# Kernel optimization log

Measured on AMD Instinct MI355X. Metric: run time of the kernel, lower is better.

Reference implementation:

```python
import jax, jax.numpy as jnp
import numpy as np

GRID_SIZE = 5
SPLINE_ORDER = 3
GRID_RANGE = (-1.0, 1.0)
BN_EPS = 1e-5


def _make_grid():
    h = (GRID_RANGE[1] - GRID_RANGE[0]) / GRID_SIZE
    # grid_size + 2*spline_order + 1 = 12 knots, shared across the 9 patch features
    return jnp.arange(-SPLINE_ORDER, GRID_SIZE + SPLINE_ORDER + 1, dtype=jnp.float32) * h + GRID_RANGE[0]


def _b_splines(x, grid):
    # x: (N, F) -> (N, F, grid_size + spline_order) via Cox-de Boor recursion
    x = x[..., None]
    bases = ((x >= grid[:-1]) & (x < grid[1:])).astype(x.dtype)
    for k in range(1, SPLINE_ORDER + 1):
        left = (x - grid[: -(k + 1)]) / (grid[k:-1] - grid[: -(k + 1)]) * bases[..., :-1]
        right = (grid[k + 1:] - x) / (grid[k + 1:] - grid[1:-k]) * bases[..., 1:]
        bases = left + right
    return bases


def setup_inputs() -> dict:
    key = jax.random.key(0)
    ks = jax.random.split(key, 4)
    B, C, H, W = 4, 64, 96, 96
    return {
        "x": jax.random.normal(ks[0], (B, C, H, W), dtype=jnp.float32),
        "base_weight": jax.random.normal(ks[1], (1, 9), dtype=jnp.float32) * 0.3,
        "spline_weight": jax.random.normal(ks[2], (1, 9, GRID_SIZE + SPLINE_ORDER), dtype=jnp.float32) * 0.3,
        "spline_scaler": jax.random.normal(ks[3], (1, 9), dtype=jnp.float32) * 0.3 + 1.0,
        "bn_gamma": jnp.ones((C,), dtype=jnp.float32),
        "bn_beta": jnp.zeros((C,), dtype=jnp.float32),
    }


def reference(x, base_weight, spline_weight, spline_scaler, bn_gamma, bn_beta):
    B, C, H, W = x.shape
    grid = _make_grid()
    # Per-channel depthwise 3x3 patch extraction (pad 1, stride 1), shared KANLinear(9 -> 1)
    patches = jax.lax.conv_general_dilated_patches(
        x.reshape(B * C, 1, H, W), (3, 3), (1, 1), [(1, 1), (1, 1)]
    )  # (B*C, 9, H, W)
    tok = patches.transpose(0, 2, 3, 1).reshape(-1, 9)  # (N, 9)

    base_out = jax.nn.silu(tok) @ base_weight.T  # (N, 1)
    bases = _b_splines(tok, grid)  # (N, 9, 8)
    scaled_sw = (spline_weight * spline_scaler[..., None]).reshape(1, -1)  # (1, 72)
    spline_out = bases.reshape(tok.shape[0], -1) @ scaled_sw.T  # (N, 1)

    y = (base_out + spline_out).reshape(B, C, H, W)

    # BatchNorm2d (training-mode batch statistics) + ReLU
    mean = y.mean(axis=(0, 2, 3))
    var = y.var(axis=(0, 2, 3))
    y_hat = (y - mean[None, :, None, None]) * jax.lax.rsqrt(var + BN_EPS)[None, :, None, None]
    out = jax.nn.relu(y_hat * bn_gamma[None, :, None, None] + bn_beta[None, :, None, None])
    return out
```

## Files before the change

kernel.cpp:

```cpp
#include <hip/hip_runtime.h>
#include <math.h>

#define HH 96
#define WW 96
#define CC 64
#define BB 4
#define PLANE (HH * WW)
#define NPLANES (BB * CC)
#define NPC (BB * PLANE)
#define TILE 32
#define TPL 3
#define NTILES (TPL * TPL)
#define HALO 34
#define HALO_N (HALO * HALO)
#define BLOCK 256

typedef _Float16 h2v __attribute__((ext_vector_type(2)));

static __device__ __forceinline__ float dot2h(unsigned a, unsigned b, float c) {
#if __has_builtin(__builtin_amdgcn_fdot2)
    return __builtin_amdgcn_fdot2(__builtin_bit_cast(h2v, a),
                                  __builtin_bit_cast(h2v, b), c, false);
#else
    h2v x = __builtin_bit_cast(h2v, a);
    h2v y = __builtin_bit_cast(h2v, b);
    return c + (float)x[0] * (float)y[0] + (float)x[1] * (float)y[1];
#endif
}

static __device__ __forceinline__ unsigned pk16(float a, float b) {
    return __builtin_bit_cast(unsigned, __builtin_amdgcn_cvt_pkrtz(a, b));
}


__global__ __launch_bounds__(BLOCK) void kconv_stage1(
    const float* __restrict__ x,
    const float* __restrict__ base_w,
    const float* __restrict__ spline_w,
    const float* __restrict__ spline_s,
    float* __restrict__ y,
    float2* __restrict__ part)
{
    __shared__ uint4  s_n[2][HALO_N];
    __shared__ float  s_sl[2][HALO_N];
    __shared__ unsigned s_wp[36];
    __shared__ float  s_bw[9];
    __shared__ float2 red[4];

    const int tid = threadIdx.x;

    if (tid < 36) {
        const int j = tid >> 2;
        const int k = tid & 3;
        const float sc = spline_s[j];
        s_wp[tid] = pk16(spline_w[j * 8 + 2 * k] * sc,
                         spline_w[j * 8 + 2 * k + 1] * sc);
    }
    if (tid < 9) s_bw[tid] = base_w[tid];

    const int plane = blockIdx.y;
    const int h0 = blockIdx.x * TILE;
    const float* xp = x + (size_t)plane * PLANE;

    int hy[5], hx[5];
#pragma unroll
    for (int s = 0; s < 5; ++s) {
        const int i = tid + s * BLOCK;
        const int r = i / HALO;
        hy[s] = r;
        hx[s] = i - r * HALO;
    }

    const int tx  = tid & 31;
    const int ty4 = (tid >> 5) * 4;

    float lsum = 0.0f, lsq = 0.0f;

    float v[5];
#pragma unroll
    for (int s = 0; s < 5; ++s) {
        const int gh = h0 + hy[s] - 1;
        const int gw = hx[s] - 1;
        const bool ok = (tid + s * BLOCK < HALO_N) &&
                        gh >= 0 && gh < HH && gw >= 0 && gw < WW;
        v[s] = ok ? xp[gh * WW + gw] : 0.0f;
    }
#pragma unroll
    for (int s = 0; s < 5; ++s) {
        const int i = tid + s * BLOCK;
        if (i >= HALO_N) break;
        const float vv = v[s];
        const float e  = __expf(-vv);
        const float sl = vv * __builtin_amdgcn_rcpf(1.0f + e);
        const float sp = fmaf(vv, 2.5f, 2.5f);
        const float tf = floorf(sp);
        const float u  = sp - tf;
        const int   t  = (int)tf;
        const int   m  = t >> 1;
        const bool  odd = (t & 1) != 0;
        const float w1m = 1.0f - u;
        const float u2 = u * u;
        const float u3 = u2 * u;
        const float B0 = w1m * w1m * (w1m * (1.0f / 6.0f));
        const float B3 = u2 * (u * (1.0f / 6.0f));
        const float B1 = fmaf(-u2, 1.0f, fmaf(u3, 0.5f, 2.0f / 3.0f));
        const float B2 = 1.0f - B0 - B1 - B3;
        const unsigned h01 = pk16(B0, B1);
        const unsigned h23 = pk16(B2, B3);
        unsigned n[4];
        unsigned a_prev;
        {
            const int k0 = -1 - m;
            a_prev = (k0 == 0) ? h01 : ((k0 == 1) ? h23 : 0u);
        }
#pragma unroll
        for (int d = 0; d < 4; ++d) {
            const int k0 = d - m;
            const unsigned a_cur = (k0 == 0) ? h01 : ((k0 == 1) ? h23 : 0u);
            const unsigned sh = __builtin_amdgcn_alignbit(a_cur, a_prev, 16);
            n[d] = odd ? sh : a_cur;
            a_prev = a_cur;
        }
        s_n[0][i]  = make_uint4(n[0], n[1], n[2], n[3]);
        s_sl[0][i] = sl;
    }
    __syncthreads();

    unsigned wp[36];
    float bw[9];
#pragma unroll
    for (int q = 0; q < 36; ++q)
        wp[q] = __builtin_amdgcn_readfirstlane(s_wp[q]);
#pragma unroll
    for (int q = 0; q < 9; ++q)
        bw[q] = __int_as_float(__builtin_amdgcn_readfirstlane(__float_as_int(s_bw[q])));

#pragma unroll
    for (int wt = 0; wt < TPL; ++wt) {
        const int cur = wt & 1;
        const int nxt = cur ^ 1;

        if (wt < TPL - 1) {
            const int w0n = (wt + 1) * TILE;
#pragma unroll
            for (int s = 0; s < 5; ++s) {
                const int gh = h0 + hy[s] - 1;
                const int gw = w0n + hx[s] - 1;
                const bool ok = (tid + s * BLOCK < HALO_N) &&
                                gh >= 0 && gh < HH && gw >= 0 && gw < WW;
                v[s] = ok ? xp[gh * WW + gw] : 0.0f;
            }
        }

        float acc[4] = {0.0f, 0.0f, 0.0f, 0.0f};
#pragma unroll
        for (int r = 0; r < 6; ++r) {
            const int base = (ty4 + r) * HALO + tx;
            uint4 cn[3];
            float cs[3];
#pragma unroll
            for (int dw = 0; dw < 3; ++dw) {
                cn[dw] = s_n[cur][base + dw];
                cs[dw] = s_sl[cur][base + dw];
            }
#pragma unroll
            for (int k = 0; k < 4; ++k) {
                const int dh = r - k;
                if (dh >= 0 && dh < 3) {
                    float a = acc[k];
#pragma unroll
                    for (int dw = 0; dw < 3; ++dw) {
                        const int j = dh * 3 + dw;
                        a = dot2h(cn[dw].x, wp[j * 4 + 0], a);
                        a = dot2h(cn[dw].y, wp[j * 4 + 1], a);
                        a = dot2h(cn[dw].z, wp[j * 4 + 2], a);
                        a = dot2h(cn[dw].w, wp[j * 4 + 3], a);
                        a = fmaf(bw[j], cs[dw], a);
                    }
                    acc[k] = a;
                }
            }
        }

        float* yp = y + (size_t)plane * PLANE + (size_t)h0 * WW + wt * TILE;
#pragma unroll
        for (int k = 0; k < 4; ++k) {
            yp[(ty4 + k) * WW + tx] = acc[k];
            lsum += acc[k];
            lsq = fmaf(acc[k], acc[k], lsq);
        }

        if (wt < TPL - 1) {
#pragma unroll
            for (int s = 0; s < 5; ++s) {
                const int i = tid + s * BLOCK;
                if (i >= HALO_N) break;
                const float vv = v[s];
                const float e  = __expf(-vv);
                const float sl = vv * __builtin_amdgcn_rcpf(1.0f + e);
                const float sp = fmaf(vv, 2.5f, 2.5f);
                const float tf = floorf(sp);
                const float u  = sp - tf;
                const int   t  = (int)tf;
                const int   m  = t >> 1;
                const bool  odd = (t & 1) != 0;
                const float w1m = 1.0f - u;
                const float u2 = u * u;
                const float u3 = u2 * u;
                const float B0 = w1m * w1m * (w1m * (1.0f / 6.0f));
                const float B3 = u2 * (u * (1.0f / 6.0f));
                const float B1 = fmaf(-u2, 1.0f, fmaf(u3, 0.5f, 2.0f / 3.0f));
                const float B2 = 1.0f - B0 - B1 - B3;
                const unsigned h01 = pk16(B0, B1);
                const unsigned h23 = pk16(B2, B3);
                unsigned n[4];
                unsigned a_prev;
                {
                    const int k0 = -1 - m;
                    a_prev = (k0 == 0) ? h01 : ((k0 == 1) ? h23 : 0u);
                }
#pragma unroll
                for (int d = 0; d < 4; ++d) {
                    const int k0 = d - m;
                    const unsigned a_cur = (k0 == 0) ? h01 : ((k0 == 1) ? h23 : 0u);
                    const unsigned sh = __builtin_amdgcn_alignbit(a_cur, a_prev, 16);
                    n[d] = odd ? sh : a_cur;
                    a_prev = a_cur;
                }
                s_n[nxt][i]  = make_uint4(n[0], n[1], n[2], n[3]);
                s_sl[nxt][i] = sl;
            }
            __syncthreads();
        }
    }

#pragma unroll
    for (int off = 32; off; off >>= 1) {
        lsum += __shfl_down(lsum, off, 64);
        lsq  += __shfl_down(lsq,  off, 64);
    }
    if ((tid & 63) == 0) red[tid >> 6] = make_float2(lsum, lsq);
    __syncthreads();
    if (tid == 0) {
        const float s = red[0].x + red[1].x + red[2].x + red[3].x;
        const float q = red[0].y + red[1].y + red[2].y + red[3].y;
        part[plane * NTILES + blockIdx.x] = make_float2(s, q);
    }
}

__global__ __launch_bounds__(BLOCK) void kconv_stage2(
    float* __restrict__ y,
    const float2* __restrict__ part,
    const float* __restrict__ gamma,
    const float* __restrict__ beta)
{
    __shared__ float2 sb;
    const int tid = threadIdx.x;
    const int plane = blockIdx.x;
    const int c = plane & (CC - 1);

    if (tid < 64) {
        float s = 0.0f, q = 0.0f;
        if (tid < 12) {
            const int b = tid / 3;
            const int t = tid - b * 3;
            const float2 pp = part[(c + CC * b) * NTILES + t];
            s = pp.x; q = pp.y;
        }
#pragma unroll
        for (int off = 8; off; off >>= 1) {
            s += __shfl_down(s, off, 64);
            q += __shfl_down(q, off, 64);
        }
        if (tid == 0) {
            const float inv = 1.0f / (float)NPC;
            const float mean = s * inv;
            const float var  = q * inv - mean * mean;
            const float sc   = rsqrtf(var + 1e-5f) * gamma[c];
            sb = make_float2(sc, beta[c] - mean * sc);
        }
    }
    __syncthreads();
    const float2 sbv = sb;

    float4* yp = (float4*)(y + (size_t)plane * PLANE + (size_t)blockIdx.y * 1024);
    float4 v = yp[tid];
    v.x = fmaxf(fmaf(v.x, sbv.x, sbv.y), 0.0f);
    v.y = fmaxf(fmaf(v.y, sbv.x, sbv.y), 0.0f);
    v.z = fmaxf(fmaf(v.z, sbv.x, sbv.y), 0.0f);
    v.w = fmaxf(fmaf(v.w, sbv.x, sbv.y), 0.0f);
    yp[tid] = v;
}

extern "C" void kernel_launch(void* const* d_in, const int* in_sizes, int n_in,
                              void* d_out, int out_size, void* d_ws, size_t ws_size,
                              hipStream_t stream)
{
    const float* x        = (const float*)d_in[0];
    const float* base_w   = (const float*)d_in[1];
    const float* spline_w = (const float*)d_in[2];
    const float* spline_s = (const float*)d_in[3];
    const float* gamma    = (const float*)d_in[4];
    const float* beta     = (const float*)d_in[5];
    float* out   = (float*)d_out;
    float2* part = (float2*)d_ws;

    dim3 g1(TPL, NPLANES);
    kconv_stage1<<<g1, BLOCK, 0, stream>>>(x, base_w, spline_w, spline_s, out, part);

    dim3 g2(NPLANES, PLANE / (BLOCK * 4));
    kconv_stage2<<<g2, BLOCK, 0, stream>>>(out, part, gamma, beta);
}
```

Measured before the change: 86.07 us.

## Fuse conv and batchnorm stages with grid-wide atomic barrier, keeping outputs in registers

Merges the two kernels into one persistent launch. Each block keeps its computed tile values in registers, publishes partial sums, and spins on a global atomic counter until all 768 blocks arrive. It then applies the batchnorm scale and shift plus ReLU and writes the output once. This removes the intermediate y write and re-read plus a kernel launch, but adds a memset launch and relies on all blocks being co-resident, with a spin timeout that could give wrong results if they are not.

```diff
diff --git a/kernel.cpp b/kernel.cpp
--- a/kernel.cpp
+++ b/kernel.cpp
@@ -10,10 +10,10 @@
 #define NPC (BB * PLANE)
 #define TILE 32
 #define TPL 3
-#define NTILES (TPL * TPL)
 #define HALO 34
 #define HALO_N (HALO * HALO)
 #define BLOCK 256
+#define NBLK (TPL * NPLANES)
 
 typedef _Float16 h2v __attribute__((ext_vector_type(2)));
 
@@ -33,19 +33,23 @@
 }
 
 
-__global__ __launch_bounds__(BLOCK) void kconv_stage1(
+__global__ __launch_bounds__(BLOCK, 3) void kconv_fused(
     const float* __restrict__ x,
     const float* __restrict__ base_w,
     const float* __restrict__ spline_w,
     const float* __restrict__ spline_s,
-    float* __restrict__ y,
-    float2* __restrict__ part)
+    const float* __restrict__ gamma,
+    const float* __restrict__ beta,
+    float* __restrict__ out,
+    float2* __restrict__ part,
+    unsigned* __restrict__ bar)
 {
     __shared__ uint4  s_n[2][HALO_N];
     __shared__ float  s_sl[2][HALO_N];
     __shared__ unsigned s_wp[36];
     __shared__ float  s_bw[9];
     __shared__ float2 red[4];
+    __shared__ float2 sb;
 
     const int tid = threadIdx.x;
 
@@ -75,6 +79,7 @@
     const int ty4 = (tid >> 5) * 4;
 
     float lsum = 0.0f, lsq = 0.0f;
+    float accAll[TPL][4];
 
     float v[5];
 #pragma unroll
@@ -182,10 +187,9 @@
             }
         }
 
-        float* yp = y + (size_t)plane * PLANE + (size_t)h0 * WW + wt * TILE;
 #pragma unroll
         for (int k = 0; k < 4; ++k) {
-            yp[(ty4 + k) * WW + tx] = acc[k];
+            accAll[wt][k] = acc[k];
             lsum += acc[k];
             lsq = fmaf(acc[k], acc[k], lsq);
         }
@@ -241,30 +245,35 @@
     }
     if ((tid & 63) == 0) red[tid >> 6] = make_float2(lsum, lsq);
     __syncthreads();
+
     if (tid == 0) {
         const float s = red[0].x + red[1].x + red[2].x + red[3].x;
         const float q = red[0].y + red[1].y + red[2].y + red[3].y;
-        part[plane * NTILES + blockIdx.x] = make_float2(s, q);
-    }
-}
-
-__global__ __launch_bounds__(BLOCK) void kconv_stage2(
-    float* __restrict__ y,
-    const float2* __restrict__ part,
-    const float* __restrict__ gamma,
-    const float* __restrict__ beta)
-{
-    __shared__ float2 sb;
-    const int tid = threadIdx.x;
-    const int plane = blockIdx.x;
+        const float2 pv = make_float2(s, q);
+        __hip_atomic_store((unsigned long long*)&part[plane * TPL + blockIdx.x],
+                           __builtin_bit_cast(unsigned long long, pv),
+                           __ATOMIC_RELAXED, __HIP_MEMORY_SCOPE_AGENT);
+        __hip_atomic_fetch_add(bar, 1u, __ATOMIC_RELEASE,
+                               __HIP_MEMORY_SCOPE_AGENT);
+        int spins = 0;
+        while (__hip_atomic_load(bar, __ATOMIC_ACQUIRE,
+                                 __HIP_MEMORY_SCOPE_AGENT) < (unsigned)NBLK) {
+            __builtin_amdgcn_s_sleep(1);
+            if (++spins > (1 << 18)) break;
+        }
+    }
+    __syncthreads();
+
     const int c = plane & (CC - 1);
-
     if (tid < 64) {
         float s = 0.0f, q = 0.0f;
         if (tid < 12) {
             const int b = tid / 3;
             const int t = tid - b * 3;
-            const float2 pp = part[(c + CC * b) * NTILES + t];
+            const unsigned long long pv = __hip_atomic_load(
+                (const unsigned long long*)&part[(c + CC * b) * TPL + t],
+                __ATOMIC_ACQUIRE, __HIP_MEMORY_SCOPE_AGENT);
+            const float2 pp = __builtin_bit_cast(float2, pv);
             s = pp.x; q = pp.y;
         }
 #pragma unroll
@@ -273,7 +282,7 @@
             q += __shfl_down(q, off, 64);
         }
         if (tid == 0) {
-            const float inv = 1.0f / (float)NPC;
+            const float inv  = 1.0f / (float)NPC;
             const float mean = s * inv;
             const float var  = q * inv - mean * mean;
             const float sc   = rsqrtf(var + 1e-5f) * gamma[c];
@@ -283,13 +292,15 @@
     __syncthreads();
     const float2 sbv = sb;
 
-    float4* yp = (float4*)(y + (size_t)plane * PLANE + (size_t)blockIdx.y * 1024);
-    float4 v = yp[tid];
-    v.x = fmaxf(fmaf(v.x, sbv.x, sbv.y), 0.0f);
-    v.y = fmaxf(fmaf(v.y, sbv.x, sbv.y), 0.0f);
-    v.z = fmaxf(fmaf(v.z, sbv.x, sbv.y), 0.0f);
-    v.w = fmaxf(fmaf(v.w, sbv.x, sbv.y), 0.0f);
-    yp[tid] = v;
+    float* yp = out + (size_t)plane * PLANE + (size_t)h0 * WW;
+#pragma unroll
+    for (int wt = 0; wt < TPL; ++wt) {
+#pragma unroll
+        for (int k = 0; k < 4; ++k) {
+            yp[(ty4 + k) * WW + wt * TILE + tx] =
+                fmaxf(fmaf(accAll[wt][k], sbv.x, sbv.y), 0.0f);
+        }
+    }
 }
 
 extern "C" void kernel_launch(void* const* d_in, const int* in_sizes, int n_in,
@@ -304,10 +315,11 @@
     const float* beta     = (const float*)d_in[5];
     float* out   = (float*)d_out;
     float2* part = (float2*)d_ws;
+    unsigned* bar = (unsigned*)((char*)d_ws + 8192);
+
+    hipMemsetAsync(bar, 0, 16, stream);
 
     dim3 g1(TPL, NPLANES);
-    kconv_stage1<<<g1, BLOCK, 0, stream>>>(x, base_w, spline_w, spline_s, out, part);
-
-    dim3 g2(NPLANES, PLANE / (BLOCK * 4));
-    kconv_stage2<<<g2, BLOCK, 0, stream>>>(out, part, gamma, beta);
+    kconv_fused<<<g1, BLOCK, 0, stream>>>(x, base_w, spline_w, spline_s,
+                                          gamma, beta, out, part, bar);
 }
```

Result: slower. 183.6 us (+113.4%).

## Split stage1 into one block per 32x32 tile, dropping double-buffered loop

Applied to the files above, without the earlier changes.

Stage 1 previously ran one block per 32-row strip that walked three 32-wide tiles, double-buffering the halo in LDS so the next tile's loads overlapped compute. Now each block handles a single tile, giving 2304 blocks instead of 768, with half the shared memory and no inner loop or intermediate syncs. Stage 2 reduces 36 partials per channel instead of 12. The change trades the software pipelining for more parallelism and occupancy, at the cost of extra block launch and per-block setup overhead.

```diff
diff --git a/kernel.cpp b/kernel.cpp
--- a/kernel.cpp
+++ b/kernel.cpp
@@ -9,8 +9,8 @@
 #define NPLANES (BB * CC)
 #define NPC (BB * PLANE)
 #define TILE 32
-#define TPL 3
-#define NTILES (TPL * TPL)
+#define TPT 3
+#define NTILES (TPT * TPT)
 #define HALO 34
 #define HALO_N (HALO * HALO)
 #define BLOCK 256
@@ -41,8 +41,8 @@
     float* __restrict__ y,
     float2* __restrict__ part)
 {
-    __shared__ uint4  s_n[2][HALO_N];
-    __shared__ float  s_sl[2][HALO_N];
+    __shared__ uint4  s_n[HALO_N];
+    __shared__ float  s_sl[HALO_N];
     __shared__ unsigned s_wp[36];
     __shared__ float  s_bw[9];
     __shared__ float2 red[4];
@@ -59,10 +59,13 @@
     if (tid < 9) s_bw[tid] = base_w[tid];
 
     const int plane = blockIdx.y;
-    const int h0 = blockIdx.x * TILE;
+    const int t  = blockIdx.x;
+    const int r0 = (t / TPT) * TILE;
+    const int c0 = (t - (t / TPT) * TPT) * TILE;
     const float* xp = x + (size_t)plane * PLANE;
 
     int hy[5], hx[5];
+    float v[5];
 #pragma unroll
     for (int s = 0; s < 5; ++s) {
         const int i = tid + s * BLOCK;
@@ -70,21 +73,15 @@
         hy[s] = r;
         hx[s] = i - r * HALO;
     }
-
-    const int tx  = tid & 31;
-    const int ty4 = (tid >> 5) * 4;
-
-    float lsum = 0.0f, lsq = 0.0f;
-
-    float v[5];
 #pragma unroll
     for (int s = 0; s < 5; ++s) {
-        const int gh = h0 + hy[s] - 1;
-        const int gw = hx[s] - 1;
+        const int gh = r0 + hy[s] - 1;
+        const int gw = c0 + hx[s] - 1;
         const bool ok = (tid + s * BLOCK < HALO_N) &&
                         gh >= 0 && gh < HH && gw >= 0 && gw < WW;
         v[s] = ok ? xp[gh * WW + gw] : 0.0f;
     }
+
 #pragma unroll
     for (int s = 0; s < 5; ++s) {
         const int i = tid + s * BLOCK;
@@ -95,9 +92,9 @@
         const float sp = fmaf(vv, 2.5f, 2.5f);
         const float tf = floorf(sp);
         const float u  = sp - tf;
-        const int   t  = (int)tf;
-        const int   m  = t >> 1;
-        const bool  odd = (t & 1) != 0;
+        const int   tt = (int)tf;
+        const int   m  = tt >> 1;
+        const bool  odd = (tt & 1) != 0;
         const float w1m = 1.0f - u;
         const float u2 = u * u;
         const float u3 = u2 * u;
@@ -121,8 +118,8 @@
             n[d] = odd ? sh : a_cur;
             a_prev = a_cur;
         }
-        s_n[0][i]  = make_uint4(n[0], n[1], n[2], n[3]);
-        s_sl[0][i] = sl;
+        s_n[i]  = make_uint4(n[0], n[1], n[2], n[3]);
+        s_sl[i] = sl;
     }
     __syncthreads();
 
@@ -135,103 +132,46 @@
     for (int q = 0; q < 9; ++q)
         bw[q] = __int_as_float(__builtin_amdgcn_readfirstlane(__float_as_int(s_bw[q])));
 
-#pragma unroll
-    for (int wt = 0; wt < TPL; ++wt) {
-        const int cur = wt & 1;
-        const int nxt = cur ^ 1;
-
-        if (wt < TPL - 1) {
-            const int w0n = (wt + 1) * TILE;
-#pragma unroll
-            for (int s = 0; s < 5; ++s) {
-                const int gh = h0 + hy[s] - 1;
-                const int gw = w0n + hx[s] - 1;
-                const bool ok = (tid + s * BLOCK < HALO_N) &&
-                                gh >= 0 && gh < HH && gw >= 0 && gw < WW;
-                v[s] = ok ? xp[gh * WW + gw] : 0.0f;
+    const int tx  = tid & 31;
+    const int ty4 = (tid >> 5) * 4;
+
+    float acc[4] = {0.0f, 0.0f, 0.0f, 0.0f};
+#pragma unroll
+    for (int r = 0; r < 6; ++r) {
+        const int base = (ty4 + r) * HALO + tx;
+        uint4 cn[3];
+        float cs[3];
+#pragma unroll
+        for (int dw = 0; dw < 3; ++dw) {
+            cn[dw] = s_n[base + dw];
+            cs[dw] = s_sl[base + dw];
+        }
+#pragma unroll
+        for (int k = 0; k < 4; ++k) {
+            const int dh = r - k;
+            if (dh >= 0 && dh < 3) {
+                float a = acc[k];
+#pragma unroll
+                for (int dw = 0; dw < 3; ++dw) {
+                    const int j = dh * 3 + dw;
+                    a = dot2h(cn[dw].x, wp[j * 4 + 0], a);
+                    a = dot2h(cn[dw].y, wp[j * 4 + 1], a);
+                    a = dot2h(cn[dw].z, wp[j * 4 + 2], a);
+                    a = dot2h(cn[dw].w, wp[j * 4 + 3], a);
+                    a = fmaf(bw[j], cs[dw], a);
+                }
+                acc[k] = a;
             }
         }
-
-        float acc[4] = {0.0f, 0.0f, 0.0f, 0.0f};
-#pragma unroll
-        for (int r = 0; r < 6; ++r) {
-            const int base = (ty4 + r) * HALO + tx;
-            uint4 cn[3];
-            float cs[3];
-#pragma unroll
-            for (int dw = 0; dw < 3; ++dw) {
-                cn[dw] = s_n[cur][base + dw];
-                cs[dw] = s_sl[cur][base + dw];
-            }
-#pragma unroll
-            for (int k = 0; k < 4; ++k) {
-                const int dh = r - k;
-                if (dh >= 0 && dh < 3) {
-                    float a = acc[k];
-#pragma unroll
-                    for (int dw = 0; dw < 3; ++dw) {
-                        const int j = dh * 3 + dw;
-                        a = dot2h(cn[dw].x, wp[j * 4 + 0], a);
-                        a = dot2h(cn[dw].y, wp[j * 4 + 1], a);
-                        a = dot2h(cn[dw].z, wp[j * 4 + 2], a);
-                        a = dot2h(cn[dw].w, wp[j * 4 + 3], a);
-                        a = fmaf(bw[j], cs[dw], a);
-                    }
-                    acc[k] = a;
-                }
-            }
-        }
-
-        float* yp = y + (size_t)plane * PLANE + (size_t)h0 * WW + wt * TILE;
-#pragma unroll
-        for (int k = 0; k < 4; ++k) {
-            yp[(ty4 + k) * WW + tx] = acc[k];
-            lsum += acc[k];
-            lsq = fmaf(acc[k], acc[k], lsq);
-        }
-
-        if (wt < TPL - 1) {
-#pragma unroll
-            for (int s = 0; s < 5; ++s) {
-                const int i = tid + s * BLOCK;
-                if (i >= HALO_N) break;
-                const float vv = v[s];
-                const float e  = __expf(-vv);
-                const float sl = vv * __builtin_amdgcn_rcpf(1.0f + e);
-                const float sp = fmaf(vv, 2.5f, 2.5f);
-                const float tf = floorf(sp);
-                const float u  = sp - tf;
-                const int   t  = (int)tf;
-                const int   m  = t >> 1;
-                const bool  odd = (t & 1) != 0;
-                const float w1m = 1.0f - u;
-                const float u2 = u * u;
-                const float u3 = u2 * u;
-                const float B0 = w1m * w1m * (w1m * (1.0f / 6.0f));
-                const float B3 = u2 * (u * (1.0f / 6.0f));
-                const float B1 = fmaf(-u2, 1.0f, fmaf(u3, 0.5f, 2.0f / 3.0f));
-                const float B2 = 1.0f - B0 - B1 - B3;
-                const unsigned h01 = pk16(B0, B1);
-                const unsigned h23 = pk16(B2, B3);
-                unsigned n[4];
-                unsigned a_prev;
-                {
-                    const int k0 = -1 - m;
-                    a_prev = (k0 == 0) ? h01 : ((k0 == 1) ? h23 : 0u);
-                }
-#pragma unroll
-                for (int d = 0; d < 4; ++d) {
-                    const int k0 = d - m;
-                    const unsigned a_cur = (k0 == 0) ? h01 : ((k0 == 1) ? h23 : 0u);
-                    const unsigned sh = __builtin_amdgcn_alignbit(a_cur, a_prev, 16);
-                    n[d] = odd ? sh : a_cur;
-                    a_prev = a_cur;
-                }
-                s_n[nxt][i]  = make_uint4(n[0], n[1], n[2], n[3]);
-                s_sl[nxt][i] = sl;
-            }
-            __syncthreads();
-        }
+    }
+
+    float lsum = 0.0f, lsq = 0.0f;
+    float* yp = y + (size_t)plane * PLANE + (size_t)r0 * WW + c0;
+#pragma unroll
+    for (int k = 0; k < 4; ++k) {
+        yp[(ty4 + k) * WW + tx] = acc[k];
+        lsum += acc[k];
+        lsq = fmaf(acc[k], acc[k], lsq);
     }
 
 #pragma unroll
@@ -244,7 +184,7 @@
     if (tid == 0) {
         const float s = red[0].x + red[1].x + red[2].x + red[3].x;
         const float q = red[0].y + red[1].y + red[2].y + red[3].y;
-        part[plane * NTILES + blockIdx.x] = make_float2(s, q);
+        part[plane * NTILES + t] = make_float2(s, q);
     }
 }
 
@@ -261,14 +201,14 @@
 
     if (tid < 64) {
         float s = 0.0f, q = 0.0f;
-        if (tid < 12) {
-            const int b = tid / 3;
-            const int t = tid - b * 3;
+        if (tid < 36) {
+            const int b = tid / 9;
+            const int t = tid - b * 9;
             const float2 pp = part[(c + CC * b) * NTILES + t];
             s = pp.x; q = pp.y;
         }
 #pragma unroll
-        for (int off = 8; off; off >>= 1) {
+        for (int off = 32; off; off >>= 1) {
             s += __shfl_down(s, off, 64);
             q += __shfl_down(q, off, 64);
         }
@@ -305,7 +245,7 @@
     float* out   = (float*)d_out;
     float2* part = (float2*)d_ws;
 
-    dim3 g1(TPL, NPLANES);
+    dim3 g1(NTILES, NPLANES);
     kconv_stage1<<<g1, BLOCK, 0, stream>>>(x, base_w, spline_w, spline_s, out, part);
 
     dim3 g2(NPLANES, PLANE / (BLOCK * 4));
```

After: 86.83 us. No clear change (+0.9%).
